# Kernel tuning notes

Hardware: AMD Instinct MI355X
Metric: run time of the kernel (lower is better)

## Reference

```python
import jax, jax.numpy as jnp
import numpy as np

B, S, E, H, M, K, FF = 4, 256, 1024, 16, 65536, 32, 4096
HD = E // H
LN_EPS = 1e-5


def _ln(x, g, b):
    mu = jnp.mean(x, axis=-1, keepdims=True)
    var = jnp.var(x, axis=-1, keepdims=True)
    return (x - mu) * jax.lax.rsqrt(var + LN_EPS) * g + b


def _mha(q, k, v, wq, bq, wk, bk, wv, bv, wo, bo):
    Bq, Sq, _ = q.shape
    Sk = k.shape[1]
    Q = (q @ wq + bq).reshape(Bq, Sq, H, HD)
    Kh = (k @ wk + bk).reshape(Bq, Sk, H, HD)
    V = (v @ wv + bv).reshape(Bq, Sk, H, HD)
    scores = jnp.einsum('bqhd,bkhd->bhqk', Q, Kh) / np.float32(np.sqrt(HD))
    attn = jax.nn.softmax(scores, axis=-1)
    out = jnp.einsum('bhqk,bkhd->bqhd', attn, V).reshape(Bq, Sq, E)
    return out @ wo + bo


def setup_inputs() -> dict:
    key = jax.random.key(0)
    ks = iter(jax.random.split(key, 16))
    d = {
        'x': jax.random.normal(next(ks), (B, S, E), jnp.float32),
        'mem_keys': jax.random.normal(next(ks), (M, E), jnp.float32),
        'mem_vals': jax.random.normal(next(ks), (M, E), jnp.float32),
    }
    for p in ('sa', 'ma'):
        for w in ('wq', 'wk', 'wv', 'wo'):
            d[f'{p}_{w}'] = 0.02 * jax.random.normal(next(ks), (E, E), jnp.float32)
        for bname in ('bq', 'bk', 'bv', 'bo'):
            d[f'{p}_{bname}'] = jnp.zeros((E,), jnp.float32)
    for ln in ('ln1', 'ln2', 'ln3'):
        d[f'{ln}_g'] = jnp.ones((E,), jnp.float32)
        d[f'{ln}_b'] = jnp.zeros((E,), jnp.float32)
    d['fc1_w'] = 0.02 * jax.random.normal(next(ks), (E, FF), jnp.float32)
    d['fc1_b'] = jnp.zeros((FF,), jnp.float32)
    d['fc2_w'] = 0.02 * jax.random.normal(next(ks), (FF, E), jnp.float32)
    d['fc2_b'] = jnp.zeros((E,), jnp.float32)
    return d


def reference(x, mem_keys, mem_vals,
              sa_wq, sa_bq, sa_wk, sa_bk, sa_wv, sa_bv, sa_wo, sa_bo,
              ma_wq, ma_bq, ma_wk, ma_bk, ma_wv, ma_bv, ma_wo, ma_bo,
              ln1_g, ln1_b, ln2_g, ln2_b, ln3_g, ln3_b,
              fc1_w, fc1_b, fc2_w, fc2_b):
    # self-attention block (eval mode -> dropout is identity)
    a = _mha(x, x, x, sa_wq, sa_bq, sa_wk, sa_bk, sa_wv, sa_bv, sa_wo, sa_bo)
    x1 = _ln(x + a, ln1_g, ln1_b)
    # kNN retrieval: cosine sim -> top-k -> gather values
    qn = x1 / jnp.maximum(jnp.linalg.norm(x1, axis=-1, keepdims=True), 1e-12)
    mkn = mem_keys / jnp.maximum(jnp.linalg.norm(mem_keys, axis=-1, keepdims=True), 1e-12)
    sims = jnp.einsum('bse,me->bsm', qn, mkn)              # (B,S,M)
    _, idx = jax.lax.top_k(sims, K)                        # (B,S,K)
    retrieved = mem_vals[idx]                              # (B,S,K,E)
    rflat = retrieved.reshape(B, S * K, E)
    # memory cross-attention over retrieved values
    m = _mha(x1, rflat, rflat, ma_wq, ma_bq, ma_wk, ma_bk, ma_wv, ma_bv, ma_wo, ma_bo)
    x2 = _ln(x1 + m, ln2_g, ln2_b)
    # FFN (exact GELU, as torch default)
    h = jax.nn.gelu(x2 @ fc1_w + fc1_b, approximate=False)
    y = h @ fc2_w + fc2_b
    return _ln(x2 + y, ln3_g, ln3_b)
```

## Files before the change

kernel.cpp:

```cpp
#include <hip/hip_runtime.h>
#include <hip/hip_bf16.h>
#include <math.h>

#define DEVFN __device__ __forceinline__

typedef __attribute__((ext_vector_type(8))) short bf16x8;
typedef __attribute__((ext_vector_type(8))) unsigned short u16x8;
typedef __attribute__((ext_vector_type(4))) unsigned short u16x4;
typedef __attribute__((ext_vector_type(4))) float f32x4;

static constexpr int Bn = 4, Sn = 256, En = 1024, Hn = 16;
static constexpr int Mn = 65536, Kt = 32, FFn = 4096;
static constexpr int NT = Bn * Sn;
static constexpr float QS = 0.18033688011112042f;

DEVFN unsigned short f2b(float f) {
  unsigned int u = __float_as_uint(f);
  unsigned int r = (u + 0x7FFFu + ((u >> 16) & 1u)) >> 16;
  return (unsigned short)r;
}
DEVFN float b2f(unsigned short u) { return __uint_as_float((unsigned)u << 16); }

DEVFN unsigned okey16(unsigned short u) {
  return (unsigned)(u ^ ((u >> 15) ? 0xFFFFu : 0x8000u)) & 0xFFFFu;
}

typedef const __attribute__((address_space(1))) void* as1cv_t;
typedef __attribute__((address_space(3))) void* as3v_t;
DEVFN void gload16(const void* g, void* l) {
  __builtin_amdgcn_global_load_lds((as1cv_t)g, (as3v_t)l, 16, 0, 0);
}
#define MEMFENCE asm volatile("" ::: "memory")

struct P8 { const float* s[8]; };

__global__ __launch_bounds__(256) void k_transpose8(
    P8 ps, unsigned short* __restrict__ outbase) {
  const float* in = ps.s[blockIdx.z];
  unsigned short* out = outbase + (size_t)blockIdx.z * En * En;
  __shared__ float tile[64][65];
  int tx = threadIdx.x & 63, ty = threadIdx.x >> 6;
  int c0 = blockIdx.x * 64, r0 = blockIdx.y * 64;
  #pragma unroll
  for (int i = 0; i < 16; i++) {
    int r = ty + i * 4;
    tile[tx][r] = in[(size_t)(r0 + r) * En + (c0 + tx)];
  }
  __syncthreads();
  #pragma unroll
  for (int i = 0; i < 16; i++) {
    int c = ty + i * 4;
    out[(size_t)(c0 + c) * En + (r0 + tx)] = f2b(tile[c][tx]);
  }
}

__global__ __launch_bounds__(256) void k_transpose_bf16(
    const float* __restrict__ in, unsigned short* __restrict__ out, int R, int C) {
  __shared__ float tile[64][65];
  int tx = threadIdx.x & 63, ty = threadIdx.x >> 6;
  int c0 = blockIdx.x * 64, r0 = blockIdx.y * 64;
  #pragma unroll
  for (int i = 0; i < 16; i++) {
    int r = ty + i * 4;
    tile[tx][r] = in[(size_t)(r0 + r) * C + (c0 + tx)];
  }
  __syncthreads();
  #pragma unroll
  for (int i = 0; i < 16; i++) {
    int c = ty + i * 4;
    out[(size_t)(c0 + c) * R + (r0 + tx)] = f2b(tile[c][tx]);
  }
}

__global__ __launch_bounds__(256) void k_cvt_bf16(
    const float* __restrict__ in, unsigned short* __restrict__ out, int n4) {
  int i = blockIdx.x * 256 + threadIdx.x;
  if (i >= n4) return;
  float4 v = ((const float4*)in)[i];
  uint2 o;
  o.x = (unsigned int)f2b(v.x) | ((unsigned int)f2b(v.y) << 16);
  o.y = (unsigned int)f2b(v.z) | ((unsigned int)f2b(v.w) << 16);
  ((uint2*)out)[i] = o;
}

__global__ __launch_bounds__(256) void k_gathercvt(
    const float* __restrict__ mv, const int* __restrict__ idx,
    unsigned short* __restrict__ out) {
  int r = blockIdx.x;
  int src = idx[r];
  float4 v = ((const float4*)(mv + (size_t)src * En))[threadIdx.x];
  uint2 o;
  o.x = (unsigned int)f2b(v.x) | ((unsigned int)f2b(v.y) << 16);
  o.y = (unsigned int)f2b(v.z) | ((unsigned int)f2b(v.w) << 16);
  ((uint2*)(out + (size_t)r * En))[threadIdx.x] = o;
}

__global__ __launch_bounds__(256) void k_concat3(
    const float* __restrict__ a, const float* __restrict__ b,
    const float* __restrict__ c, float* __restrict__ o) {
  int i = blockIdx.x * 256 + threadIdx.x;
  float v = (i < 1024) ? a[i] : (i < 2048) ? b[i - 1024] : c[i - 2048];
  o[i] = v;
}

__global__ __launch_bounds__(256) void k_normcvt(
    const float* __restrict__ mk, unsigned short* __restrict__ out) {
  int m = blockIdx.x, t = threadIdx.x;
  float4 v = ((const float4*)(mk + (size_t)m * En))[t];
  float ss = v.x*v.x + v.y*v.y + v.z*v.z + v.w*v.w;
  #pragma unroll
  for (int d = 32; d; d >>= 1) ss += __shfl_down(ss, d);
  __shared__ float red[4];
  int lane = t & 63, w = t >> 6;
  if (lane == 0) red[w] = ss;
  __syncthreads();
  float rs = 1.0f / fmaxf(sqrtf(red[0] + red[1] + red[2] + red[3]), 1e-12f);
  uint2 o;
  o.x = (unsigned int)f2b(v.x * rs) | ((unsigned int)f2b(v.y * rs) << 16);
  o.y = (unsigned int)f2b(v.z * rs) | ((unsigned int)f2b(v.w * rs) << 16);
  ((uint2*)(out + (size_t)m * En))[t] = o;
}

__global__ __launch_bounds__(256) void k_layernorm4(
    const float* __restrict__ pp, const float* __restrict__ pbias,
    const float* __restrict__ resid,
    const float* __restrict__ g, const float* __restrict__ bb,
    float* __restrict__ outf, unsigned short* __restrict__ outb) {
  int n = blockIdx.x, t = threadIdx.x;
  const size_t PS = (size_t)NT * En / 4;
  size_t i = (size_t)n * 256 + t;
  float4 p0 = ((const float4*)pp)[i];
  float4 p1 = ((const float4*)pp)[i + PS];
  float4 p2 = ((const float4*)pp)[i + 2 * PS];
  float4 p3 = ((const float4*)pp)[i + 3 * PS];
  float4 rv = ((const float4*)(resid + (size_t)n * En))[t];
  float4 bi = ((const float4*)pbias)[t];
  float4 v;
  v.x = (p0.x + p1.x) + (p2.x + p3.x) + bi.x + rv.x;
  v.y = (p0.y + p1.y) + (p2.y + p3.y) + bi.y + rv.y;
  v.z = (p0.z + p1.z) + (p2.z + p3.z) + bi.z + rv.z;
  v.w = (p0.w + p1.w) + (p2.w + p3.w) + bi.w + rv.w;
  float s  = v.x + v.y + v.z + v.w;
  float s2 = v.x*v.x + v.y*v.y + v.z*v.z + v.w*v.w;
  #pragma unroll
  for (int d = 32; d; d >>= 1) { s += __shfl_down(s, d); s2 += __shfl_down(s2, d); }
  __shared__ float rs[4], rq[4];
  int lane = t & 63, w = t >> 6;
  if (lane == 0) { rs[w] = s; rq[w] = s2; }
  __syncthreads();
  float mean = (rs[0]+rs[1]+rs[2]+rs[3]) * (1.0f/En);
  float var  = (rq[0]+rq[1]+rq[2]+rq[3]) * (1.0f/En) - mean*mean;
  float rstd = rsqrtf(var + 1e-5f);
  float4 gg = ((const float4*)g)[t];
  float4 bv = ((const float4*)bb)[t];
  float o0 = (v.x-mean)*rstd*gg.x + bv.x;
  float o1 = (v.y-mean)*rstd*gg.y + bv.y;
  float o2 = (v.z-mean)*rstd*gg.z + bv.z;
  float o3 = (v.w-mean)*rstd*gg.w + bv.w;
  if (outf) { float4 ov = {o0,o1,o2,o3}; ((float4*)(outf + (size_t)n*En))[t] = ov; }
  if (outb) {
    uint2 o;
    o.x = (unsigned int)f2b(o0) | ((unsigned int)f2b(o1) << 16);
    o.y = (unsigned int)f2b(o2) | ((unsigned int)f2b(o3) << 16);
    ((uint2*)(outb + (size_t)n*En))[t] = o;
  }
}

template<int EPI, int NOUT, int LSWZ>
__global__ __launch_bounds__(512) void k_gemm256(
    const unsigned short* __restrict__ Ab, const unsigned short* __restrict__ Bb,
    const float* __restrict__ bias,
    float* __restrict__ Cf, unsigned short* __restrict__ cb0, unsigned short* __restrict__ cb1,
    int Ndim, int Kdim, int nRT, int nCT) {
  extern __shared__ unsigned short lds[];
  const int t = threadIdx.x, lane = t & 63, w = t >> 6;
  const int wr = w >> 2, wc = w & 3, l15 = lane & 15, l4 = lane >> 4;
  const int lr2 = lane >> 2;
  const int cg  = (lane & 3) ^ (((lane >> 5) & 1) << 1);

  const int nwg = nRT * nCT;
  int lb = ((int)blockIdx.x % 8) * (nwg >> 3) + ((int)blockIdx.x >> 3);
  int rowT, colT;
  if (LSWZ == 0) { rowT = lb % nRT; colT = lb / nRT; }
  else           { colT = lb % nCT; rowT = lb / nCT; }
  const int row0 = rowT * 256, col0 = colT * 256;

  auto pa = [&](int h) -> unsigned short* { return lds + h * 16384; };
  auto pb = [&](int h) -> unsigned short* { return lds + h * 16384 + 8192; };

  const unsigned short* aSrc0 = Ab + (size_t)(row0 + w * 32 + lr2) * Kdim + cg * 8;
  const unsigned short* aSrc1 = aSrc0 + (size_t)16 * Kdim;
  const unsigned short* bSrc0 = Bb + (size_t)(col0 + w * 32 + lr2) * Kdim + cg * 8;
  const unsigned short* bSrc1 = bSrc0 + (size_t)16 * Kdim;

  f32x4 acc[8][4];
  #pragma unroll
  for (int i = 0; i < 8; i++)
    #pragma unroll
    for (int j = 0; j < 4; j++) acc[i][j] = (f32x4){0.f, 0.f, 0.f, 0.f};

  const int NH = Kdim >> 5;
  #pragma unroll
  for (int h = 0; h < 3; ++h) {
    const int ko = h * 32;
    gload16(aSrc0 + ko, pa(h) + w*32*32);
    gload16(aSrc1 + ko, pa(h) + (w*32+16)*32);
    gload16(bSrc0 + ko, pb(h) + w*32*32);
    gload16(bSrc1 + ko, pb(h) + (w*32+16)*32);
  }
  asm volatile("s_waitcnt vmcnt(8)" ::: "memory");
  __builtin_amdgcn_s_barrier();
  MEMFENCE;

  for (int hs = 0; hs < NH; ++hs) {
    const int cur = hs & 3;
    const unsigned short* Ap = pa(cur);
    const unsigned short* Bp = pb(cur);
    const int h3 = (hs + 3) & 3, ko3 = (hs + 3) * 32;
    const bool pf = (hs + 3) < NH;
    bf16x8 bfr[4], af[4];

    #pragma unroll
    for (int ni = 0; ni < 4; ni++) {
      int row = wc * 64 + ni * 16 + l15;
      int c8 = l4 ^ (((row >> 3) & 1) << 1);
      bfr[ni] = *(const bf16x8*)&Bp[row * 32 + c8 * 8];
    }
    #pragma unroll
    for (int m = 0; m < 4; m++) {
      int row = wr * 128 + m * 16 + l15;
      int c8 = l4 ^ (((row >> 3) & 1) << 1);
      af[m] = *(const bf16x8*)&Ap[row * 32 + c8 * 8];
    }
    if (pf) {
      gload16(aSrc0 + ko3, pa(h3) + w*32*32);
      gload16(aSrc1 + ko3, pa(h3) + (w*32+16)*32);
    }
    __builtin_amdgcn_s_setprio(1);
    #pragma unroll
    for (int m = 0; m < 4; m++)
      #pragma unroll
      for (int ni = 0; ni < 4; ni++)
        acc[m][ni] = __builtin_amdgcn_mfma_f32_16x16x32_bf16(af[m], bfr[ni], acc[m][ni], 0, 0, 0);
    __builtin_amdgcn_s_setprio(0);

    #pragma unroll
    for (int m = 0; m < 4; m++) {
      int row = wr * 128 + (4 + m) * 16 + l15;
      int c8 = l4 ^ (((row >> 3) & 1) << 1);
      af[m] = *(const bf16x8*)&Ap[row * 32 + c8 * 8];
    }
    if (pf) {
      gload16(bSrc0 + ko3, pb(h3) + w*32*32);
      gload16(bSrc1 + ko3, pb(h3) + (w*32+16)*32);
    }
    __builtin_amdgcn_s_setprio(1);
    #pragma unroll
    for (int m = 0; m < 4; m++)
      #pragma unroll
      for (int ni = 0; ni < 4; ni++)
        acc[4 + m][ni] = __builtin_amdgcn_mfma_f32_16x16x32_bf16(af[m], bfr[ni], acc[4 + m][ni], 0, 0, 0);
    __builtin_amdgcn_s_setprio(0);

    if (hs + 1 < NH) {
      const int rem = NH - 2 - hs;
      if (rem >= 2)      asm volatile("s_waitcnt vmcnt(8)" ::: "memory");
      else if (rem == 1) asm volatile("s_waitcnt vmcnt(4)" ::: "memory");
      else               asm volatile("s_waitcnt vmcnt(0)" ::: "memory");
      __builtin_amdgcn_s_barrier();
      MEMFENCE;
    }
  }

  #pragma unroll
  for (int m = 0; m < 8; m++) {
    #pragma unroll
    for (int ni = 0; ni < 4; ni++) {
      int col  = col0 + wc * 64 + ni * 16 + l15;
      int rowb = row0 + wr * 128 + m * 16 + l4 * 4;
      if constexpr (EPI == 6) {
        if (col < 1024) {
          #pragma unroll
          for (int r = 0; r < 4; r++)
            cb0[(size_t)(rowb + r) * 1024 + col] = f2b(acc[m][ni][r] + bias[col]);
        } else {
          int c = col - 1024;
          int bi = rowb >> 13, k0 = rowb & 8191;
          u16x4 o;
          #pragma unroll
          for (int r = 0; r < 4; r++) o[r] = f2b(acc[m][ni][r] + bias[col]);
          *(u16x4*)&cb1[((size_t)bi * 1024 + c) * 8192 + k0] = o;
        }
      } else {
        #pragma unroll
        for (int r = 0; r < 4; r++)
          cb0[(size_t)(rowb + r) * Ndim + col] = f2b(acc[m][ni][r]);
      }
    }
  }
}

template<int EPI, int NOUT, bool QSC, int SK>
__global__ __launch_bounds__(256) void k_gemm(
    const unsigned short* __restrict__ Ab, const unsigned short* __restrict__ Bb,
    const float* __restrict__ bias,
    float* __restrict__ Cf, unsigned short* __restrict__ cb0,
    unsigned short* __restrict__ cb1, unsigned short* __restrict__ cb2,
    int Ndim, int Kdim) {
  __shared__ unsigned short ring[3][2][128 * 32];
  const int t = threadIdx.x, lane = t & 63, w = t >> 6;
  const int wr = w >> 1, wc = w & 1, l15 = lane & 15, l4 = lane >> 4;
  const int lr2 = lane >> 2;
  const int cg  = (lane & 3) ^ (((lane >> 5) & 1) << 1);
  const int row0 = blockIdx.y * 128;
  const int col0 = blockIdx.x * 128;
  const int koff = (SK > 1) ? (int)blockIdx.z * (Kdim / SK) : 0;
  const int NH = ((SK > 1) ? (Kdim / SK) : Kdim) >> 5;

  const unsigned short* aSrc0 = Ab + (size_t)(row0 + w * 32 + lr2) * Kdim + koff + cg * 8;
  const unsigned short* aSrc1 = aSrc0 + (size_t)16 * Kdim;
  const unsigned short* bSrc0 = Bb + (size_t)(col0 + w * 32 + lr2) * Kdim + koff + cg * 8;
  const unsigned short* bSrc1 = bSrc0 + (size_t)16 * Kdim;

  f32x4 acc[4][4];
  #pragma unroll
  for (int i = 0; i < 4; i++)
    #pragma unroll
    for (int j = 0; j < 4; j++) acc[i][j] = (f32x4){0.f,0.f,0.f,0.f};

  auto stage = [&](int h, int buf) {
    const int ko = h * 32;
    gload16(aSrc0 + ko, &ring[buf][0][w * 32 * 32]);
    gload16(aSrc1 + ko, &ring[buf][0][(w * 32 + 16) * 32]);
    gload16(bSrc0 + ko, &ring[buf][1][w * 32 * 32]);
    gload16(bSrc1 + ko, &ring[buf][1][(w * 32 + 16) * 32]);
  };

  stage(0, 0);
  stage(1, 1);
  asm volatile("s_waitcnt vmcnt(4)" ::: "memory");
  __builtin_amdgcn_s_barrier();
  MEMFENCE;

  int cur = 0;
  for (int hs = 0; hs < NH; ++hs) {
    const unsigned short* Ap = &ring[cur][0][0];
    const unsigned short* Bp = &ring[cur][1][0];
    bf16x8 af[4], bfr[4];
    #pragma unroll
    for (int ni = 0; ni < 4; ni++) {
      int row = wc * 64 + ni * 16 + l15;
      int c8 = l4 ^ (((row >> 3) & 1) << 1);
      bfr[ni] = *(const bf16x8*)&Bp[row * 32 + c8 * 8];
    }
    #pragma unroll
    for (int m = 0; m < 4; m++) {
      int row = wr * 64 + m * 16 + l15;
      int c8 = l4 ^ (((row >> 3) & 1) << 1);
      af[m] = *(const bf16x8*)&Ap[row * 32 + c8 * 8];
    }
    if (hs + 2 < NH) {
      int nb = cur + 2; if (nb >= 3) nb -= 3;
      stage(hs + 2, nb);
    }
    __builtin_amdgcn_s_setprio(1);
    #pragma unroll
    for (int mi = 0; mi < 4; mi++)
      #pragma unroll
      for (int ni = 0; ni < 4; ni++)
        acc[mi][ni] = __builtin_amdgcn_mfma_f32_16x16x32_bf16(af[mi], bfr[ni], acc[mi][ni], 0, 0, 0);
    __builtin_amdgcn_s_setprio(0);
    if (hs + 1 < NH) {
      if (hs + 2 < NH) asm volatile("s_waitcnt vmcnt(4)" ::: "memory");
      else             asm volatile("s_waitcnt vmcnt(0)" ::: "memory");
      __builtin_amdgcn_s_barrier();
      MEMFENCE;
    }
    cur = cur + 1; if (cur >= 3) cur -= 3;
  }

  unsigned short* cbase = cb0;
  int colsub = 0;
  float qsc = 1.0f;
  if constexpr (NOUT > 1) {
    int which = col0 >> 10;
    cbase = (which == 0) ? cb0 : (which == 1) ? cb1 : cb2;
    colsub = col0 & 1023;
    if (QSC && which == 0) qsc = QS;
  } else if constexpr (QSC) {
    qsc = QS;
  }
  float* Cfp = Cf;
  if constexpr (EPI == 7) Cfp = Cf + (size_t)blockIdx.z * NT * En;

  #pragma unroll
  for (int mi = 0; mi < 4; mi++) {
    #pragma unroll
    for (int ni = 0; ni < 4; ni++) {
      int col  = col0 + wc*64 + ni*16 + l15;
      int rowb = row0 + wr*64 + mi*16 + l4*4;
      #pragma unroll
      for (int r = 0; r < 4; r++) {
        float v = acc[mi][ni][r];
        size_t off = (size_t)(rowb + r) * Ndim + col;
        if constexpr (EPI == 0) {
          if constexpr (NOUT > 1) {
            int c2 = colsub + wc*64 + ni*16 + l15;
            cbase[(size_t)(rowb + r) * 1024 + c2] = f2b((v + bias[col]) * qsc);
          } else {
            cb0[off] = f2b((v + bias[col]) * qsc);
          }
        } else if constexpr (EPI == 2) {
          float u = v + bias[col];
          u = 0.5f * u * (1.0f + erff(u * 0.70710678118654752f));
          cb0[off] = f2b(u);
        } else if constexpr (EPI == 7) {
          Cfp[off] = v;
        } else {
          Cf[off] = v;
        }
      }
    }
  }
}

__global__ __launch_bounds__(256) void k_attn_sa(
    const unsigned short* __restrict__ Qp, const unsigned short* __restrict__ Kp,
    const unsigned short* __restrict__ Vp, unsigned short* __restrict__ Op, int Lk) {
  __shared__ unsigned short Ks[64][72];
  __shared__ unsigned short Vt[64][72];
  __shared__ float Ps[4][16][68];
  const int b = blockIdx.z;
  const int h = blockIdx.y, q0 = blockIdx.x * 64;
  const int t = threadIdx.x, lane = t & 63, w = t >> 6;
  const int l15 = lane & 15, l4 = lane >> 4;

  const int qrow = q0 + w * 16 + l15;
  const unsigned short* qptr = Qp + (size_t)(b * Sn + qrow) * En + h * 64 + l4 * 8;
  bf16x8 qf0 = *(const bf16x8*)qptr;
  bf16x8 qf1 = *(const bf16x8*)(qptr + 32);

  f32x4 oacc[4];
  #pragma unroll
  for (int i = 0; i < 4; i++) oacc[i] = (f32x4){0.f,0.f,0.f,0.f};
  float m_[4] = {-INFINITY, -INFINITY, -INFINITY, -INFINITY};
  float l_[4] = {0.f, 0.f, 0.f, 0.f};

  const int nkt = Lk / 64;
  for (int kt = 0; kt < nkt; ++kt) {
    __syncthreads();
    #pragma unroll
    for (int i = 0; i < 2; i++) {
      int ld = t + i * 256;
      int kr = ld >> 3, d8 = (ld & 7) * 8;
      size_t base = (size_t)(b * Lk + kt * 64 + kr) * En + h * 64 + d8;
      *(uint4*)&Ks[kr][d8] = *(const uint4*)(Kp + base);
      bf16x8 vv = *(const bf16x8*)(Vp + base);
      int colswz = kr ^ ((t & 7) << 3);
      #pragma unroll
      for (int j = 0; j < 8; j++) Vt[d8 + j][colswz] = ((unsigned short*)&vv)[j];
    }
    __syncthreads();

    f32x4 s[4];
    #pragma unroll
    for (int ni = 0; ni < 4; ni++) {
      s[ni] = (f32x4){0.f,0.f,0.f,0.f};
      bf16x8 kb0 = *(const bf16x8*)&Ks[ni*16 + l15][l4*8];
      bf16x8 kb1 = *(const bf16x8*)&Ks[ni*16 + l15][l4*8 + 32];
      s[ni] = __builtin_amdgcn_mfma_f32_16x16x32_bf16(qf0, kb0, s[ni], 0, 0, 0);
      s[ni] = __builtin_amdgcn_mfma_f32_16x16x32_bf16(qf1, kb1, s[ni], 0, 0, 0);
    }

    #pragma unroll
    for (int r = 0; r < 4; r++) {
      float mx = fmaxf(fmaxf(s[0][r], s[1][r]), fmaxf(s[2][r], s[3][r]));
      #pragma unroll
      for (int d2 = 1; d2 < 16; d2 <<= 1) mx = fmaxf(mx, __shfl_xor(mx, d2));
      float m = m_[r];
      if (mx > m + 8.f) {
        float alpha = exp2f(m - mx);
        l_[r] *= alpha;
        #pragma unroll
        for (int nd = 0; nd < 4; nd++) oacc[nd][r] *= alpha;
        m = mx; m_[r] = mx;
      }
      float p0 = exp2f(s[0][r] - m), p1 = exp2f(s[1][r] - m);
      float p2 = exp2f(s[2][r] - m), p3 = exp2f(s[3][r] - m);
      s[0][r] = p0; s[1][r] = p1; s[2][r] = p2; s[3][r] = p3;
      l_[r] += (p0 + p1) + (p2 + p3);
    }

    #pragma unroll
    for (int ni = 0; ni < 4; ni++)
      #pragma unroll
      for (int r = 0; r < 4; r++)
        Ps[w][l4*4 + r][ni*16 + l15] = s[ni][r];
    asm volatile("s_waitcnt lgkmcnt(0)" ::: "memory");

    #pragma unroll
    for (int half = 0; half < 2; half++) {
      float4 pv0 = *(const float4*)&Ps[w][l15][half*32 + l4*8];
      float4 pv1 = *(const float4*)&Ps[w][l15][half*32 + l4*8 + 4];
      bf16x8 pa;
      pa[0]=(short)f2b(pv0.x); pa[1]=(short)f2b(pv0.y); pa[2]=(short)f2b(pv0.z); pa[3]=(short)f2b(pv0.w);
      pa[4]=(short)f2b(pv1.x); pa[5]=(short)f2b(pv1.y); pa[6]=(short)f2b(pv1.z); pa[7]=(short)f2b(pv1.w);
      #pragma unroll
      for (int nd = 0; nd < 4; nd++) {
        int dd = nd*16 + l15;
        bf16x8 vb = *(const bf16x8*)&Vt[dd][(half*32 + l4*8) ^ (((dd >> 3) & 7) << 3)];
        oacc[nd] = __builtin_amdgcn_mfma_f32_16x16x32_bf16(pa, vb, oacc[nd], 0, 0, 0);
      }
    }
  }

  #pragma unroll
  for (int r = 0; r < 4; r++) {
    float lv = l_[r];
    #pragma unroll
    for (int d2 = 1; d2 < 16; d2 <<= 1) lv += __shfl_xor(lv, d2);
    l_[r] = lv;
  }
  #pragma unroll
  for (int nd = 0; nd < 4; nd++)
    #pragma unroll
    for (int r = 0; r < 4; r++) {
      int q = q0 + w*16 + l4*4 + r;
      Op[(size_t)(b * Sn + q) * En + h * 64 + nd*16 + l15] = f2b(oacc[nd][r] / l_[r]);
    }
}

__global__ __launch_bounds__(256, 2) void k_attn_ma(
    const unsigned short* __restrict__ Qp, const unsigned short* __restrict__ Kp,
    const unsigned short* __restrict__ Vp,
    unsigned short* __restrict__ PO, float* __restrict__ PM, float* __restrict__ PL) {
  constexpr int Lk = Sn * Kt;
  constexpr int NTI = 8;
  __shared__ unsigned short Ks[2][64 * 64];
  __shared__ unsigned short Vt[2][64 * 64];
  __shared__ float Ps[4][16][68];
  const int sp = blockIdx.x, h = blockIdx.y, b = blockIdx.z;
  const int t = threadIdx.x, lane = t & 63, w = t >> 6;
  const int l15 = lane & 15, l4 = lane >> 4;
  const int l8 = lane >> 3, l7 = lane & 7;
  const int kswz = (l7 ^ l8) * 8;
  const int rbase = w * 16;

  bf16x8 qf[4][2];
  #pragma unroll
  for (int qt = 0; qt < 4; qt++) {
    const unsigned short* qptr = Qp + (size_t)(b * Sn + w * 64 + qt * 16 + l15) * En + h * 64 + l4 * 8;
    qf[qt][0] = *(const bf16x8*)qptr;
    qf[qt][1] = *(const bf16x8*)(qptr + 32);
  }

  f32x4 oacc[4][4];
  #pragma unroll
  for (int i = 0; i < 4; i++)
    #pragma unroll
    for (int j = 0; j < 4; j++) oacc[i][j] = (f32x4){0.f,0.f,0.f,0.f};
  float m_[4][4], l_[4][4];
  #pragma unroll
  for (int i = 0; i < 4; i++)
    #pragma unroll
    for (int j = 0; j < 4; j++) { m_[i][j] = -INFINITY; l_[i][j] = 0.f; }

  const int kt0 = sp * NTI;
  auto stage = [&](int kt, int buf) {
    #pragma unroll
    for (int i = 0; i < 2; i++) {
      int row = rbase + i * 8 + l8;
      gload16(Kp + (size_t)(b * Lk + kt * 64 + row) * En + h * 64 + kswz,
              &Ks[buf][(rbase + i * 8) * 64]);
      gload16(Vp + ((size_t)b * 1024 + h * 64 + row) * (size_t)Lk + kt * 64 + kswz,
              &Vt[buf][(rbase + i * 8) * 64]);
    }
  };

  stage(kt0, 0);
  stage(kt0 + 1, 1);
  asm volatile("s_waitcnt vmcnt(4)" ::: "memory");
  __builtin_amdgcn_s_barrier();
  MEMFENCE;

  for (int j = 0; j < NTI; ++j) {
    const int cur = j & 1;
    #pragma unroll
    for (int qt = 0; qt < 4; qt++) {
      f32x4 s[4];
      #pragma unroll
      for (int ni = 0; ni < 4; ni++) {
        s[ni] = (f32x4){0.f,0.f,0.f,0.f};
        int rowK = ni * 16 + l15, sw = (rowK & 7) * 8;
        bf16x8 kb0 = *(const bf16x8*)&Ks[cur][rowK * 64 + ((l4 * 8) ^ sw)];
        bf16x8 kb1 = *(const bf16x8*)&Ks[cur][rowK * 64 + ((l4 * 8 + 32) ^ sw)];
        s[ni] = __builtin_amdgcn_mfma_f32_16x16x32_bf16(qf[qt][0], kb0, s[ni], 0, 0, 0);
        s[ni] = __builtin_amdgcn_mfma_f32_16x16x32_bf16(qf[qt][1], kb1, s[ni], 0, 0, 0);
      }
      #pragma unroll
      for (int r = 0; r < 4; r++) {
        float mx = fmaxf(fmaxf(s[0][r], s[1][r]), fmaxf(s[2][r], s[3][r]));
        #pragma unroll
        for (int d2 = 1; d2 < 16; d2 <<= 1) mx = fmaxf(mx, __shfl_xor(mx, d2));
        float m = m_[qt][r];
        if (mx > m + 8.f) {
          float alpha = exp2f(m - mx);
          l_[qt][r] *= alpha;
          #pragma unroll
          for (int nd = 0; nd < 4; nd++) oacc[qt][nd][r] *= alpha;
          m = mx; m_[qt][r] = mx;
        }
        float p0 = exp2f(s[0][r] - m), p1 = exp2f(s[1][r] - m);
        float p2 = exp2f(s[2][r] - m), p3 = exp2f(s[3][r] - m);
        s[0][r] = p0; s[1][r] = p1; s[2][r] = p2; s[3][r] = p3;
        l_[qt][r] += (p0 + p1) + (p2 + p3);
      }
      #pragma unroll
      for (int ni = 0; ni < 4; ni++)
        #pragma unroll
        for (int r = 0; r < 4; r++)
          Ps[w][l4*4 + r][ni*16 + l15] = s[ni][r];
      asm volatile("s_waitcnt lgkmcnt(0)" ::: "memory");
      #pragma unroll
      for (int half = 0; half < 2; half++) {
        float4 pv0 = *(const float4*)&Ps[w][l15][half*32 + l4*8];
        float4 pv1 = *(const float4*)&Ps[w][l15][half*32 + l4*8 + 4];
        bf16x8 pa;
        pa[0]=(short)f2b(pv0.x); pa[1]=(short)f2b(pv0.y); pa[2]=(short)f2b(pv0.z); pa[3]=(short)f2b(pv0.w);
        pa[4]=(short)f2b(pv1.x); pa[5]=(short)f2b(pv1.y); pa[6]=(short)f2b(pv1.z); pa[7]=(short)f2b(pv1.w);
        #pragma unroll
        for (int nd = 0; nd < 4; nd++) {
          int dd = nd*16 + l15;
          bf16x8 vb = *(const bf16x8*)&Vt[cur][dd * 64 + ((half*32 + l4*8) ^ ((dd & 7) * 8))];
          oacc[qt][nd] = __builtin_amdgcn_mfma_f32_16x16x32_bf16(pa, vb, oacc[qt][nd], 0, 0, 0);
        }
      }
    }
    MEMFENCE; __builtin_amdgcn_s_barrier(); MEMFENCE;
    if (j + 2 < NTI) stage(kt0 + j + 2, cur);
    if (j + 1 < NTI) {
      if (j + 2 < NTI) asm volatile("s_waitcnt vmcnt(4)" ::: "memory");
      else             asm volatile("s_waitcnt vmcnt(0)" ::: "memory");
      __builtin_amdgcn_s_barrier();
      MEMFENCE;
    }
  }

  #pragma unroll
  for (int qt = 0; qt < 4; qt++)
    #pragma unroll
    for (int r = 0; r < 4; r++) {
      float lv = l_[qt][r];
      #pragma unroll
      for (int d2 = 1; d2 < 16; d2 <<= 1) lv += __shfl_xor(lv, d2);
      l_[qt][r] = lv;
    }

  const int slot = (b * Hn + h) * 16 + sp;
  #pragma unroll
  for (int qt = 0; qt < 4; qt++)
    #pragma unroll
    for (int nd = 0; nd < 4; nd++)
      #pragma unroll
      for (int r = 0; r < 4; r++)
        PO[(size_t)slot * 16384 + (w*64 + qt*16 + l4*4 + r) * 64 + nd*16 + l15] = f2b(oacc[qt][nd][r]);
  if (l15 == 0) {
    #pragma unroll
    for (int qt = 0; qt < 4; qt++)
      #pragma unroll
      for (int r = 0; r < 4; r++) {
        PM[slot * 256 + w*64 + qt*16 + l4*4 + r] = m_[qt][r];
        PL[slot * 256 + w*64 + qt*16 + l4*4 + r] = l_[qt][r];
      }
  }
}

__global__ __launch_bounds__(256) void k_attn_comb16(
    const unsigned short* __restrict__ PO, const float* __restrict__ PM,
    const float* __restrict__ PL, unsigned short* __restrict__ Op) {
  const int W = blockIdx.x * 4 + (threadIdx.x >> 6);
  const int lane = threadIdx.x & 63;
  const int bh = W >> 8, q = W & 255;
  const int slotBase = bh * 16;
  float ms[16];
  float M = -INFINITY;
  #pragma unroll
  for (int s = 0; s < 16; s++) { ms[s] = PM[(slotBase + s) * 256 + q]; M = fmaxf(M, ms[s]); }
  float L = 0.f, acc = 0.f;
  #pragma unroll
  for (int s = 0; s < 16; s++) {
    float wgt = exp2f(ms[s] - M);
    L += PL[(slotBase + s) * 256 + q] * wgt;
    acc += wgt * b2f(PO[(size_t)(slotBase + s) * 16384 + q * 64 + lane]);
  }
  const int b = bh >> 4, h = bh & 15;
  Op[(size_t)(b * Sn + q) * En + h * 64 + lane] = f2b(acc / L);
}

DEVFN unsigned blk_exscan16(unsigned part, volatile unsigned* wsum, int lane, int wid) {
  unsigned v = part;
  #pragma unroll
  for (int d = 1; d < 64; d <<= 1) { unsigned o = __shfl_up(v, d); if (lane >= d) v += o; }
  if (lane == 63) wsum[wid] = v;
  __syncthreads();
  unsigned woff = 0;
  for (int i = 0; i < wid; i++) woff += wsum[i];
  unsigned r = woff + v - part;
  __syncthreads();
  return r;
}

DEVFN void find_thr16(const unsigned* hist, int NB, unsigned need,
                      int t, int lane, int wid, volatile unsigned* wsum,
                      volatile int* s_thr, volatile unsigned* s_above) {
  int per = NB >> 10;
  int lo = NB - per * (t + 1);
  unsigned part = 0;
  for (int j = 0; j < per; j++) part += hist[lo + j];
  unsigned ex = blk_exscan16(part, wsum, lane, wid);
  if (ex < need && ex + part >= need) {
    unsigned c = ex;
    for (int j = per - 1; j >= 0; j--) {
      unsigned h = hist[lo + j];
      if (c + h >= need) { *s_thr = lo + j; *s_above = c; break; }
      c += h;
    }
  }
  __syncthreads();
}

__global__ __launch_bounds__(1024) void k_topk16(
    const unsigned short* __restrict__ simsb, int* __restrict__ oidx) {
  const int n = blockIdx.x, t = threadIdx.x;
  const int lane = t & 63, wid = t >> 6;
  const u16x8* row8 = (const u16x8*)(simsb + (size_t)n * Mn);
  constexpr unsigned CAP = 2048;
  __shared__ unsigned hist[2048];
  __shared__ unsigned wsum[16];
  __shared__ int s_thr;
  __shared__ unsigned s_above;
  __shared__ unsigned h2[32];
  __shared__ unsigned s_cnt, s_na;
  __shared__ unsigned short ckey[CAP];
  __shared__ unsigned cidx[CAP];
  __shared__ int slist[32];
  __shared__ unsigned sL, sneedEq, scntEq, s_imin;

  for (int i = t; i < 2048; i += 1024) hist[i] = 0;
  if (t < 32) h2[t] = 0;
  if (t == 0) { s_cnt = 0; s_na = 0; }
  __syncthreads();

  {
    u16x8 v = row8[3584 + t];
    #pragma unroll
    for (int j = 0; j < 8; j++) atomicAdd(&hist[okey16(v[j]) >> 5], 1u);
  }
  __syncthreads();
  find_thr16(hist, 2048, 32, t, lane, wid, wsum, &s_thr, &s_above);
  const unsigned base = ((unsigned)s_thr) << 5;

  #pragma unroll
  for (int p = 0; p < 8; p++) {
    u16x8 v = row8[p * 1024 + t];
    unsigned i0 = (unsigned)(p * 1024 + t) * 8;
    #pragma unroll
    for (int j = 0; j < 8; j++) {
      unsigned k = okey16(v[j]);
      if (k >= base) {
        unsigned slot = atomicAdd(&s_cnt, 1u);
        if (slot < CAP) { ckey[slot] = (unsigned short)k; cidx[slot] = i0 + j; }
      }
    }
  }
  __syncthreads();
  const unsigned total = s_cnt;

  unsigned L, istar = 0xFFFFFFFFu;
  if (total <= CAP) {
    for (int i = t; i < 2048; i += 1024) hist[i] = 0;
    __syncthreads();
    for (unsigned i = t; i < total; i += 1024)
      atomicAdd(&hist[(unsigned)ckey[i] >> 5], 1u);
    __syncthreads();
    find_thr16(hist, 2048, 32, t, lane, wid, wsum, &s_thr, &s_above);
    const unsigned T1 = (unsigned)s_thr;
    const unsigned need2 = 32 - s_above;
    const unsigned cnt1 = hist[T1];
    if (cnt1 == need2) {
      L = T1 << 5;
    } else {
      for (unsigned i = t; i < total; i += 1024) {
        unsigned k = (unsigned)ckey[i];
        if ((k >> 5) == T1) atomicAdd(&h2[k & 31], 1u);
      }
      __syncthreads();
      if (t == 0) {
        unsigned cum = 0; int T3 = 0; unsigned above = 0;
        for (int j = 31; j >= 0; j--) {
          if (cum + h2[j] >= need2) { T3 = j; above = cum; break; }
          cum += h2[j];
        }
        sL = (T1 << 5) | (unsigned)T3;
        sneedEq = need2 - above;
        scntEq = h2[T3];
      }
      __syncthreads();
      L = sL;
      if (scntEq != sneedEq) {
        int prev = -1;
        for (unsigned j = 0; j < sneedEq; j++) {
          if (t == 0) s_imin = 0xFFFFFFFFu;
          __syncthreads();
          for (unsigned i = t; i < total; i += 1024)
            if ((unsigned)ckey[i] == L && (int)cidx[i] > prev) atomicMin(&s_imin, cidx[i]);
          __syncthreads();
          prev = (int)s_imin;
          __syncthreads();
        }
        istar = (unsigned)prev;
      }
    }
    __syncthreads();
    for (unsigned i = t; i < total; i += 1024) {
      unsigned k = (unsigned)ckey[i];
      if (k > L || (k == L && cidx[i] <= istar)) {
        unsigned s = atomicAdd(&s_na, 1u);
        slist[s] = (int)cidx[i];
      }
    }
    __syncthreads();
    if (t < 32) {
      int my = slist[t];
      int rank = 0;
      #pragma unroll
      for (int j = 0; j < 32; j++) rank += (slist[j] < my);
      oidx[n * Kt + rank] = my;
    }
  } else {
    for (int i = t; i < 2048; i += 1024) hist[i] = 0;
    __syncthreads();
    #pragma unroll
    for (int p = 0; p < 8; p++) {
      u16x8 v = row8[p * 1024 + t];
      #pragma unroll
      for (int j = 0; j < 8; j++) atomicAdd(&hist[okey16(v[j]) >> 5], 1u);
    }
    __syncthreads();
    find_thr16(hist, 2048, 32, t, lane, wid, wsum, &s_thr, &s_above);
    const unsigned T1 = (unsigned)s_thr;
    const unsigned need2 = 32 - s_above;
    const unsigned cnt1 = hist[T1];
    if (cnt1 == need2) {
      L = T1 << 5;
    } else {
      for (int p = 0; p < 8; p++) {
        u16x8 v = row8[p * 1024 + t];
        #pragma unroll
        for (int j = 0; j < 8; j++) {
          unsigned k = okey16(v[j]);
          if ((k >> 5) == T1) atomicAdd(&h2[k & 31], 1u);
        }
      }
      __syncthreads();
      if (t == 0) {
        unsigned cum = 0; int T3 = 0; unsigned above = 0;
        for (int j = 31; j >= 0; j--) {
          if (cum + h2[j] >= need2) { T3 = j; above = cum; break; }
          cum += h2[j];
        }
        sL = (T1 << 5) | (unsigned)T3;
        sneedEq = need2 - above;
        scntEq = h2[T3];
      }
      __syncthreads();
      L = sL;
      if (scntEq != sneedEq) {
        const unsigned short* rowp = simsb + (size_t)n * Mn;
        unsigned cntLoc = 0;
        for (int j = 0; j < 64; j++)
          if (okey16(rowp[t * 64 + j]) == L) cntLoc++;
        unsigned pre = blk_exscan16(cntLoc, wsum, lane, wid);
        unsigned c = 0;
        for (int j = 0; j < 64; j++)
          if (okey16(rowp[t * 64 + j]) == L) { if (pre + c < 32) slist[pre + c] = t * 64 + j; c++; }
        __syncthreads();
        istar = (unsigned)slist[sneedEq - 1];
        __syncthreads();
      }
    }
    __syncthreads();
    unsigned cnt = 0;
    for (int p = 0; p < 8; p++) {
      u16x8 v = row8[p * 1024 + t];
      unsigned i0 = (unsigned)(p * 1024 + t) * 8;
      #pragma unroll
      for (int j = 0; j < 8; j++) {
        unsigned k = okey16(v[j]);
        cnt += (k > L || (k == L && i0 + j <= istar));
      }
    }
    unsigned pos = blk_exscan16(cnt, wsum, lane, wid);
    for (int p = 0; p < 8; p++) {
      u16x8 v = row8[p * 1024 + t];
      unsigned i0 = (unsigned)(p * 1024 + t) * 8;
      #pragma unroll
      for (int j = 0; j < 8; j++) {
        unsigned k = okey16(v[j]);
        if (k > L || (k == L && i0 + j <= istar)) oidx[n * Kt + pos++] = (int)(i0 + j);
      }
    }
  }
}

extern "C" void kernel_launch(void* const* d_in, const int* in_sizes, int n_in,
                              void* d_out, int out_size, void* d_ws, size_t ws_size,
                              hipStream_t stream) {
  (void)in_sizes; (void)n_in; (void)out_size;
  const float* x      = (const float*)d_in[0];
  const float* mem_k  = (const float*)d_in[1];
  const float* mem_v  = (const float*)d_in[2];
  const float* sa_w[4] = {(const float*)d_in[3], (const float*)d_in[4], (const float*)d_in[5], (const float*)d_in[6]};
  const float* sa_b[4] = {(const float*)d_in[7], (const float*)d_in[8], (const float*)d_in[9], (const float*)d_in[10]};
  const float* ma_w[4] = {(const float*)d_in[11], (const float*)d_in[12], (const float*)d_in[13], (const float*)d_in[14]};
  const float* ma_b[4] = {(const float*)d_in[15], (const float*)d_in[16], (const float*)d_in[17], (const float*)d_in[18]};
  const float* ln_g[3] = {(const float*)d_in[19], (const float*)d_in[21], (const float*)d_in[23]};
  const float* ln_b[3] = {(const float*)d_in[20], (const float*)d_in[22], (const float*)d_in[24]};
  const float* fc1_w = (const float*)d_in[25];
  const float* fc1_b = (const float*)d_in[26];
  const float* fc2_w = (const float*)d_in[27];
  const float* fc2_b = (const float*)d_in[28];
  float* out = (float*)d_out;

  char* ws = (char*)d_ws;
  size_t off = 0;
  auto alloc = [&](size_t bytes) -> char* {
    char* p = ws + off;
    off = (off + bytes + 255) & ~(size_t)255;
    return p;
  };

  unsigned short* wt[8];
  for (int i = 0; i < 8; i++) wt[i] = (unsigned short*)alloc((size_t)En * En * 2);
  unsigned short* fc1t  = (unsigned short*)alloc((size_t)FFn * En * 2);
  unsigned short* fc2t  = (unsigned short*)alloc((size_t)En * FFn * 2);
  unsigned short* xb    = (unsigned short*)alloc((size_t)NT * En * 2);
  unsigned short* Qb    = (unsigned short*)alloc((size_t)NT * En * 2);
  unsigned short* Kb    = (unsigned short*)alloc((size_t)NT * En * 2);
  unsigned short* Vb    = (unsigned short*)alloc((size_t)NT * En * 2);
  unsigned short* at1b  = (unsigned short*)alloc((size_t)NT * En * 2);
  float*          x1f   = (float*)alloc((size_t)NT * En * 4);
  unsigned short* x1b   = (unsigned short*)alloc((size_t)NT * En * 2);
  char*           simsRaw = alloc((size_t)NT * Mn * 4);
  int*            idx   = (int*)alloc((size_t)NT * Kt * 4);
  unsigned short* K2b   = (unsigned short*)alloc((size_t)NT * Kt * En * 2);
  unsigned short* V2b   = (unsigned short*)alloc((size_t)NT * Kt * En * 2);
  unsigned short* Q2b   = (unsigned short*)alloc((size_t)NT * En * 2);
  unsigned short* at2b  = (unsigned short*)alloc((size_t)NT * En * 2);
  float*          x2f   = (float*)alloc((size_t)NT * En * 4);
  unsigned short* x2b   = (unsigned short*)alloc((size_t)NT * En * 2);
  unsigned short* hb    = (unsigned short*)alloc((size_t)NT * FFn * 2);
  float*          pp    = (float*)alloc((size_t)4 * NT * En * 4);
  float*          bcat_sa = (float*)alloc(3072 * 4);
  float*          bcat_ma = (float*)alloc(2048 * 4);

  if (off > ws_size) return;

  unsigned short* simsb = (unsigned short*)simsRaw;
  unsigned short* mkb = (unsigned short*)K2b;
  unsigned short* Ab2 = (unsigned short*)(simsRaw + (size_t)128 * 1024 * 1024);
  unsigned short* PO  = (unsigned short*)(simsRaw + (size_t)192 * 1024 * 1024);
  float* PM = (float*)(simsRaw + (size_t)224 * 1024 * 1024);
  float* PL = (float*)(simsRaw + (size_t)225 * 1024 * 1024);

  (void)hipFuncSetAttribute((const void*)&k_gemm256<5,1,0>,
                            hipFuncAttributeMaxDynamicSharedMemorySize, 131072);
  (void)hipFuncSetAttribute((const void*)&k_gemm256<6,2,1>,
                            hipFuncAttributeMaxDynamicSharedMemorySize, 131072);

  P8 p8;
  for (int i = 0; i < 4; i++) { p8.s[i] = sa_w[i]; p8.s[4 + i] = ma_w[i]; }
  k_transpose8<<<dim3(16, 16, 8), 256, 0, stream>>>(p8, wt[0]);
  k_transpose_bf16<<<dim3(64, 16), 256, 0, stream>>>(fc1_w, fc1t, En, FFn);
  k_transpose_bf16<<<dim3(16, 64), 256, 0, stream>>>(fc2_w, fc2t, FFn, En);
  k_concat3<<<dim3(12), 256, 0, stream>>>(sa_b[0], sa_b[1], sa_b[2], bcat_sa);
  k_concat3<<<dim3(8),  256, 0, stream>>>(ma_b[1], ma_b[2], ma_b[2], bcat_ma);

  k_cvt_bf16<<<dim3(NT * En / 4 / 256), 256, 0, stream>>>(x, xb, NT * En / 4);
  k_normcvt<<<dim3(Mn), 256, 0, stream>>>(mem_k, mkb);

  const dim3 g1(En / 128, NT / 128);
  const dim3 g1s(En / 128, NT / 128, 4);

  k_gemm<0,3,true,1><<<dim3(24, 8), 256, 0, stream>>>(xb, wt[0], bcat_sa, nullptr, Qb, Kb, Vb, 3072, En);
  k_attn_sa<<<dim3(Sn / 64, Hn, Bn), 256, 0, stream>>>(Qb, Kb, Vb, at1b, Sn);
  k_gemm<7,1,false,4><<<g1s, 256, 0, stream>>>(at1b, wt[3], nullptr, pp, nullptr, nullptr, nullptr, En, En);
  k_layernorm4<<<NT, 256, 0, stream>>>(pp, sa_b[3], x, ln_g[0], ln_b[0], x1f, x1b);

  k_gemm256<5,1,0><<<dim3(1024), 512, 131072, stream>>>(
      x1b, mkb, nullptr, nullptr, simsb, nullptr, Mn, En, NT / 256, Mn / 256);
  k_topk16<<<NT, 1024, 0, stream>>>(simsb, idx);

  k_gathercvt<<<dim3(NT * Kt), 256, 0, stream>>>(mem_v, idx, Ab2);
  k_gemm256<6,2,1><<<dim3(1024), 512, 131072, stream>>>(
      Ab2, wt[5], bcat_ma, nullptr, K2b, V2b, 2048, En, NT * Kt / 256, 2048 / 256);
  k_gemm<0,1,true,1><<<g1, 256, 0, stream>>>(x1b, wt[4], ma_b[0], nullptr, Q2b, nullptr, nullptr, En, En);
  k_attn_ma<<<dim3(16, Hn, Bn), 256, 0, stream>>>(Q2b, K2b, V2b, PO, PM, PL);
  k_attn_comb16<<<dim3(Bn * Hn * Sn / 4), 256, 0, stream>>>(PO, PM, PL, at2b);
  k_gemm<7,1,false,4><<<g1s, 256, 0, stream>>>(at2b, wt[7], nullptr, pp, nullptr, nullptr, nullptr, En, En);
  k_layernorm4<<<NT, 256, 0, stream>>>(pp, ma_b[3], x1f, ln_g[1], ln_b[1], x2f, x2b);

  k_gemm<2,1,false,1><<<dim3(FFn / 128, NT / 128), 256, 0, stream>>>(x2b, fc1t, fc1_b, nullptr, hb, nullptr, nullptr, FFn, En);
  k_gemm<7,1,false,4><<<g1s, 256, 0, stream>>>(hb, fc2t, nullptr, pp, nullptr, nullptr, nullptr, En, FFn);
  k_layernorm4<<<NT, 256, 0, stream>>>(pp, fc2_b, x2f, ln_g[2], ln_b[2], out, nullptr);
}
```

Baseline: 749.5 us.

## Compute transposed scores in memory attention and shuffle P into registers instead of LDS

```diff
diff --git a/kernel.cpp b/kernel.cpp
--- a/kernel.cpp
+++ b/kernel.cpp
@@ -20,6 +20,12 @@
   return (unsigned short)r;
 }
 DEVFN float b2f(unsigned short u) { return __uint_as_float((unsigned)u << 16); }
+
+DEVFN unsigned cvtpk(float lo, float hi) {
+  unsigned r;
+  asm volatile("v_cvt_pk_bf16_f32 %0, %1, %2" : "=v"(r) : "v"(lo), "v"(hi));
+  return r;
+}
 
 DEVFN unsigned okey16(unsigned short u) {
   return (unsigned)(u ^ ((u >> 15) ? 0xFFFFu : 0x8000u)) & 0xFFFFu;
@@ -538,7 +544,6 @@
   constexpr int NTI = 8;
   __shared__ unsigned short Ks[2][64 * 64];
   __shared__ unsigned short Vt[2][64 * 64];
-  __shared__ float Ps[4][16][68];
   const int sp = blockIdx.x, h = blockIdx.y, b = blockIdx.z;
   const int t = threadIdx.x, lane = t & 63, w = t >> 6;
   const int l15 = lane & 15, l4 = lane >> 4;
@@ -559,11 +564,8 @@
   for (int i = 0; i < 4; i++)
     #pragma unroll
     for (int j = 0; j < 4; j++) oacc[i][j] = (f32x4){0.f,0.f,0.f,0.f};
-  float m_[4][4], l_[4][4];
-  #pragma unroll
-  for (int i = 0; i < 4; i++)
-    #pragma unroll
-    for (int j = 0; j < 4; j++) { m_[i][j] = -INFINITY; l_[i][j] = 0.f; }
+  float m_[4] = {-INFINITY, -INFINITY, -INFINITY, -INFINITY};
+  float l_[4] = {0.f, 0.f, 0.f, 0.f};
 
   const int kt0 = sp * NTI;
   auto stage = [&](int kt, int buf) {
@@ -583,6 +585,8 @@
   __builtin_amdgcn_s_barrier();
   MEMFENCE;
 
+  union PU { unsigned u[4]; bf16x8 v; };
+
   for (int j = 0; j < NTI; ++j) {
     const int cur = j & 1;
     #pragma unroll
@@ -594,45 +598,58 @@
         int rowK = ni * 16 + l15, sw = (rowK & 7) * 8;
         bf16x8 kb0 = *(const bf16x8*)&Ks[cur][rowK * 64 + ((l4 * 8) ^ sw)];
         bf16x8 kb1 = *(const bf16x8*)&Ks[cur][rowK * 64 + ((l4 * 8 + 32) ^ sw)];
-        s[ni] = __builtin_amdgcn_mfma_f32_16x16x32_bf16(qf[qt][0], kb0, s[ni], 0, 0, 0);
-        s[ni] = __builtin_amdgcn_mfma_f32_16x16x32_bf16(qf[qt][1], kb1, s[ni], 0, 0, 0);
-      }
-      #pragma unroll
-      for (int r = 0; r < 4; r++) {
-        float mx = fmaxf(fmaxf(s[0][r], s[1][r]), fmaxf(s[2][r], s[3][r]));
-        #pragma unroll
-        for (int d2 = 1; d2 < 16; d2 <<= 1) mx = fmaxf(mx, __shfl_xor(mx, d2));
-        float m = m_[qt][r];
-        if (mx > m + 8.f) {
-          float alpha = exp2f(m - mx);
-          l_[qt][r] *= alpha;
-          #pragma unroll
-          for (int nd = 0; nd < 4; nd++) oacc[qt][nd][r] *= alpha;
-          m = mx; m_[qt][r] = mx;
-        }
-        float p0 = exp2f(s[0][r] - m), p1 = exp2f(s[1][r] - m);
-        float p2 = exp2f(s[2][r] - m), p3 = exp2f(s[3][r] - m);
-        s[0][r] = p0; s[1][r] = p1; s[2][r] = p2; s[3][r] = p3;
-        l_[qt][r] += (p0 + p1) + (p2 + p3);
-      }
+        s[ni] = __builtin_amdgcn_mfma_f32_16x16x32_bf16(kb0, qf[qt][0], s[ni], 0, 0, 0);
+        s[ni] = __builtin_amdgcn_mfma_f32_16x16x32_bf16(kb1, qf[qt][1], s[ni], 0, 0, 0);
+      }
+      float mx = s[0][0];
       #pragma unroll
       for (int ni = 0; ni < 4; ni++)
         #pragma unroll
-        for (int r = 0; r < 4; r++)
-          Ps[w][l4*4 + r][ni*16 + l15] = s[ni][r];
-      asm volatile("s_waitcnt lgkmcnt(0)" ::: "memory");
+        for (int r = 0; r < 4; r++) mx = fmaxf(mx, s[ni][r]);
+      mx = fmaxf(mx, __shfl_xor(mx, 16));
+      mx = fmaxf(mx, __shfl_xor(mx, 32));
+      float mold = m_[qt];
+      bool upd = mx > mold + 8.f;
+      float mnew = upd ? mx : mold;
+      m_[qt] = mnew;
+      if (__any(upd)) {
+        float am = mold - mnew;
+        l_[qt] *= exp2f(am);
+        #pragma unroll
+        for (int r = 0; r < 4; r++) {
+          float amr = __shfl(am, (lane & 48) | (l4 * 4 + r), 64);
+          float al = exp2f(amr);
+          #pragma unroll
+          for (int nd = 0; nd < 4; nd++) oacc[qt][nd][r] *= al;
+        }
+      }
+      unsigned q32[4][2];
+      float lacc = 0.f;
+      #pragma unroll
+      for (int ni = 0; ni < 4; ni++) {
+        float p0 = exp2f(s[ni][0] - mnew), p1 = exp2f(s[ni][1] - mnew);
+        float p2 = exp2f(s[ni][2] - mnew), p3 = exp2f(s[ni][3] - mnew);
+        lacc += (p0 + p1) + (p2 + p3);
+        q32[ni][0] = cvtpk(p0, p1);
+        q32[ni][1] = cvtpk(p2, p3);
+      }
+      l_[qt] += lacc;
       #pragma unroll
       for (int half = 0; half < 2; half++) {
-        float4 pv0 = *(const float4*)&Ps[w][l15][half*32 + l4*8];
-        float4 pv1 = *(const float4*)&Ps[w][l15][half*32 + l4*8 + 4];
-        bf16x8 pa;
-        pa[0]=(short)f2b(pv0.x); pa[1]=(short)f2b(pv0.y); pa[2]=(short)f2b(pv0.z); pa[3]=(short)f2b(pv0.w);
-        pa[4]=(short)f2b(pv1.x); pa[5]=(short)f2b(pv1.y); pa[6]=(short)f2b(pv1.z); pa[7]=(short)f2b(pv1.w);
+        PU pu;
+        #pragma unroll
+        for (int wd = 0; wd < 4; wd++) {
+          int g = 2 * (l4 & 1) + (wd >> 1);
+          int src = (g << 4) | l15;
+          unsigned a0 = (unsigned)__shfl((int)q32[half * 2 + 0][wd & 1], src, 64);
+          unsigned a1 = (unsigned)__shfl((int)q32[half * 2 + 1][wd & 1], src, 64);
+          pu.u[wd] = (l4 & 2) ? a1 : a0;
+        }
         #pragma unroll
         for (int nd = 0; nd < 4; nd++) {
-          int dd = nd*16 + l15;
-          bf16x8 vb = *(const bf16x8*)&Vt[cur][dd * 64 + ((half*32 + l4*8) ^ ((dd & 7) * 8))];
-          oacc[qt][nd] = __builtin_amdgcn_mfma_f32_16x16x32_bf16(pa, vb, oacc[qt][nd], 0, 0, 0);
+          int dd = nd * 16 + l15;
+          bf16x8 vb = *(const bf16x8*)&Vt[cur][dd * 64 + ((half * 32 + l4 * 8) ^ ((dd & 7) * 8))];
+          oacc[qt][nd] = __builtin_amdgcn_mfma_f32_16x16x32_bf16(pu.v, vb, oacc[qt][nd], 0, 0, 0);
         }
       }
     }
@@ -647,14 +664,12 @@
   }
 
   #pragma unroll
-  for (int qt = 0; qt < 4; qt++)
-    #pragma unroll
-    for (int r = 0; r < 4; r++) {
-      float lv = l_[qt][r];
-      #pragma unroll
-      for (int d2 = 1; d2 < 16; d2 <<= 1) lv += __shfl_xor(lv, d2);
-      l_[qt][r] = lv;
-    }
+  for (int qt = 0; qt < 4; qt++) {
+    float lv = l_[qt];
+    lv += __shfl_xor(lv, 16);
+    lv += __shfl_xor(lv, 32);
+    l_[qt] = lv;
+  }
 
   const int slot = (b * Hn + h) * 16 + sp;
   #pragma unroll
@@ -664,14 +679,12 @@
       #pragma unroll
       for (int r = 0; r < 4; r++)
         PO[(size_t)slot * 16384 + (w*64 + qt*16 + l4*4 + r) * 64 + nd*16 + l15] = f2b(oacc[qt][nd][r]);
-  if (l15 == 0) {
-    #pragma unroll
-    for (int qt = 0; qt < 4; qt++)
-      #pragma unroll
-      for (int r = 0; r < 4; r++) {
-        PM[slot * 256 + w*64 + qt*16 + l4*4 + r] = m_[qt][r];
-        PL[slot * 256 + w*64 + qt*16 + l4*4 + r] = l_[qt][r];
-      }
+  if (lane < 16) {
+    #pragma unroll
+    for (int qt = 0; qt < 4; qt++) {
+      PM[slot * 256 + w*64 + qt*16 + l15] = m_[qt];
+      PL[slot * 256 + w*64 + qt*16 + l15] = l_[qt];
+    }
   }
 }
 
```

Measured after the change: 712.6 us. -4.9%, faster.
